# Performance work log

Hardware: AMD Instinct MI355X
Metric: run time of the kernel (lower is better)

Reference implementation:

```python
import jax, jax.numpy as jnp
import numpy as np

NEG_SLOPE_ATT = 0.2   # DenseGATConv default negative_slope
NEG_SLOPE_OUT = 0.01  # F.leaky_relu default


def dense_gat_layer(x, adj, w, att_src, att_dst, bias, heads, concat):
    # x: [B, N, F_in], adj: [B, N, N] (0/1 float), w: [F_in, H*C]
    B, N, _ = x.shape
    h = (x @ w).reshape(B, N, heads, -1)                 # [B, N, H, C]
    a_src = jnp.einsum('bnhc,hc->bnh', h, att_src)       # [B, N, H]
    a_dst = jnp.einsum('bnhc,hc->bnh', h, att_dst)       # [B, N, H]
    # alpha[b,i,j,h] = a_src[b,j,h] + a_dst[b,i,h]
    alpha = a_src[:, None, :, :] + a_dst[:, :, None, :]  # [B, N, N, H]
    alpha = jax.nn.leaky_relu(alpha, NEG_SLOPE_ATT)
    alpha = jnp.where(adj[..., None] == 0, -jnp.inf, alpha)
    alpha = jax.nn.softmax(alpha, axis=2)                # over neighbors j
    out = jnp.einsum('bijh,bjhc->bihc', alpha, h)        # [B, N, H, C]
    if concat:
        out = out.reshape(B, N, -1)                      # [B, N, H*C]
    else:
        out = out.mean(axis=2)                           # [B, N, C]
    return out + bias


def setup_inputs() -> dict:
    key = jax.random.key(0)
    ks = jax.random.split(key, 9)
    B, N, F_IN, HID, H1, OUT = 1, 4096, 256, 64, 8, 128
    x = jax.random.normal(ks[0], (B, N, F_IN), dtype=jnp.float32)
    u = jax.random.uniform(ks[1], (B, N, N), dtype=jnp.float32)
    adj = (u < 0.05).astype(jnp.float32)
    eye = jnp.eye(N, dtype=jnp.float32)[None]
    adj = jnp.maximum(adj, eye)  # ensure self-loop so softmax rows are valid
    s1 = 1.0 / np.sqrt(F_IN)
    s2 = 1.0 / np.sqrt(HID * H1)
    return {
        'x': x,
        'adj': adj,
        'w1': jax.random.normal(ks[2], (F_IN, H1 * HID), dtype=jnp.float32) * s1,
        'att_src1': jax.random.normal(ks[3], (H1, HID), dtype=jnp.float32) * s2,
        'att_dst1': jax.random.normal(ks[4], (H1, HID), dtype=jnp.float32) * s2,
        'b1': jnp.zeros((H1 * HID,), dtype=jnp.float32),
        'w2': jax.random.normal(ks[5], (H1 * HID, OUT), dtype=jnp.float32) * s2,
        'att_src2': jax.random.normal(ks[6], (1, OUT), dtype=jnp.float32) * 0.1,
        'att_dst2': jax.random.normal(ks[7], (1, OUT), dtype=jnp.float32) * 0.1,
        'b2': jnp.zeros((OUT,), dtype=jnp.float32),
    }


def reference(x, adj, w1, att_src1, att_dst1, b1, w2, att_src2, att_dst2, b2):
    h = dense_gat_layer(x, adj, w1, att_src1, att_dst1, b1, heads=8, concat=True)
    h = jax.nn.leaky_relu(h, NEG_SLOPE_OUT)
    h = dense_gat_layer(h, adj, w2, att_src2, att_dst2, b2, heads=1, concat=False)
    return jax.nn.leaky_relu(h, NEG_SLOPE_OUT)
```

## Files before the change

kernel.cpp:

```cpp
#include <hip/hip_runtime.h>
#include <hip/hip_bf16.h>
#include <cstdint>

#define N_NODES 4096
#define STRIDE  384
#define NPAIRS_MAX 192
#define WP1     196
#define QMAX    128

typedef _Float16 half2v __attribute__((ext_vector_type(2)));

__device__ __forceinline__ unsigned pkrtz(float a, float b) {
    return __builtin_bit_cast(unsigned, __builtin_amdgcn_cvt_pkrtz(a, b));
}
__device__ __forceinline__ float f16lo(unsigned u) {
    half2v h = __builtin_bit_cast(half2v, u); return (float)h.x;
}
__device__ __forceinline__ float f16hi(unsigned u) {
    half2v h = __builtin_bit_cast(half2v, u); return (float)h.y;
}
__device__ __forceinline__ unsigned pk_lo(unsigned a, unsigned b) {
    return __builtin_amdgcn_perm(b, a, 0x05040100u);
}
__device__ __forceinline__ unsigned pk_hi(unsigned a, unsigned b) {
    return __builtin_amdgcn_perm(b, a, 0x07060302u);
}
__device__ __forceinline__ float fdot2f(unsigned v, unsigned w, float acc) {
    return __builtin_amdgcn_fdot2(__builtin_bit_cast(half2v, v),
                                  __builtin_bit_cast(half2v, w), acc, false);
}
__device__ __forceinline__ float lrelu02(float s) { return (s > 0.f) ? s : 0.2f * s; }
__device__ __forceinline__ float lrelu01(float s) { return (s > 0.f) ? s : 0.01f * s; }

__global__ __launch_bounds__(256) void build_nbr_kernel(
    const float* __restrict__ adj, unsigned short* __restrict__ nbr,
    int* __restrict__ cnt, float* __restrict__ as1, float* __restrict__ ad1,
    float* __restrict__ as2, float* __restrict__ ad2) {
    const int i    = blockIdx.x;
    const int tid  = threadIdx.x;
    const int wv   = tid >> 6;
    const int lane = tid & 63;
    if (tid < 8)  { as1[i * 8 + tid] = 0.f; ad1[i * 8 + tid] = 0.f; }
    if (tid == 8) { as2[i] = 0.f; }
    if (tid == 9) { ad2[i] = 0.f; }
    __shared__ unsigned short s_buf[4][QMAX];
    __shared__ int s_cnt[4];
    const float4* row = (const float4*)(adj + (size_t)i * N_NODES);
    int base = 0;
#pragma unroll
    for (int it = 0; it < 4; it++) {
        float4 v = row[wv * 256 + it * 64 + lane];
        float e4[4] = {v.x, v.y, v.z, v.w};
        unsigned long long m4[4];
#pragma unroll
        for (int e = 0; e < 4; e++) m4[e] = __ballot(e4[e] != 0.0f);
#pragma unroll
        for (int e = 0; e < 4; e++) {
            int prefix = __popcll(m4[e] & ((1ull << lane) - 1ull));
            int pos = base + prefix;
            if (e4[e] != 0.0f && pos < QMAX)
                s_buf[wv][pos] = (unsigned short)(wv * 1024 + (it * 64 + lane) * 4 + e);
            base += __popcll(m4[e]);
        }
    }
    if (lane == 0) s_cnt[wv] = (base < QMAX) ? base : QMAX;
    __syncthreads();
    const int c0 = s_cnt[0], c1 = s_cnt[1], c2 = s_cnt[2], c3 = s_cnt[3];
    const int o1 = c0, o2 = c0 + c1, o3 = o2 + c2;
    int total = o3 + c3;
    if (total > STRIDE) total = STRIDE;
    for (int k = tid; k < total; k += 256) {
        int w, loc;
        if      (k < o1) { w = 0; loc = k; }
        else if (k < o2) { w = 1; loc = k - o1; }
        else if (k < o3) { w = 2; loc = k - o2; }
        else             { w = 3; loc = k - o3; }
        nbr[(size_t)i * STRIDE + k] = s_buf[w][loc];
    }
    if (tid == 0) cnt[i] = total;
}

template<int BM, int BN, int BK, int TM, int TN, int H>
__global__ __launch_bounds__(256) void sgemm_att_kernel(
    const float* __restrict__ A, const float* __restrict__ B,
    unsigned short* __restrict__ C16,
    const float* __restrict__ att_s, const float* __restrict__ att_d,
    float* __restrict__ as_, float* __restrict__ ad_,
    int M, int N, int K) {
    static_assert((BM / TM) * (BN / TN) == 256, "256 threads");
    static_assert(TN == 4, "epilogue assumes TN=4");
    __shared__ float As[BK][BM + 4];
    __shared__ float Bs[BK][BN + 4];
    const int tid  = threadIdx.x;
    const int tx   = tid % (BN / TN);
    const int ty   = tid / (BN / TN);
    const int row0 = blockIdx.y * BM;
    const int col0 = blockIdx.x * BN;
    float acc[TM][TN] = {};
    for (int k0 = 0; k0 < K; k0 += BK) {
        for (int i = tid; i < BM * BK / 4; i += 256) {
            int r  = i / (BK / 4);
            int kq = i % (BK / 4);
            float4 v = *(const float4*)(A + (size_t)(row0 + r) * K + k0 + kq * 4);
            As[kq * 4 + 0][r] = v.x;
            As[kq * 4 + 1][r] = v.y;
            As[kq * 4 + 2][r] = v.z;
            As[kq * 4 + 3][r] = v.w;
        }
        for (int i = tid; i < BK * BN / 4; i += 256) {
            int r  = i / (BN / 4);
            int cq = i % (BN / 4);
            *(float4*)&Bs[r][cq * 4] =
                *(const float4*)(B + (size_t)(k0 + r) * N + col0 + cq * 4);
        }
        __syncthreads();
#pragma unroll
        for (int kk = 0; kk < BK; kk++) {
            float a[TM], b[TN];
#pragma unroll
            for (int t = 0; t < TM; t++) a[t] = As[kk][ty * TM + t];
#pragma unroll
            for (int u = 0; u < TN; u++) b[u] = Bs[kk][tx * TN + u];
#pragma unroll
            for (int t = 0; t < TM; t++)
#pragma unroll
                for (int u = 0; u < TN; u++) acc[t][u] += a[t] * b[u];
        }
        __syncthreads();
    }
    float asv[TN], adv[TN];
#pragma unroll
    for (int u = 0; u < TN; u++) {
        asv[u] = att_s[col0 + tx * TN + u];
        adv[u] = att_d[col0 + tx * TN + u];
    }
    const int head = (H > 1) ? (col0 >> 6) : 0;
#pragma unroll
    for (int t = 0; t < TM; t++) {
        const int row = row0 + ty * TM + t;
        uint2 pk;
        pk.x = pkrtz(acc[t][0], acc[t][1]);
        pk.y = pkrtz(acc[t][2], acc[t][3]);
        *(uint2*)(C16 + (size_t)row * N + col0 + tx * TN) = pk;
        float ps = 0.f, pd = 0.f;
#pragma unroll
        for (int u = 0; u < TN; u++) { ps += acc[t][u] * asv[u]; pd += acc[t][u] * adv[u]; }
#pragma unroll
        for (int off = 8; off; off >>= 1) {
            ps += __shfl_xor(ps, off);
            pd += __shfl_xor(pd, off);
        }
        if (tx == 0) {
            atomicAdd(&as_[row * H + head], ps);
            atomicAdd(&ad_[row * H + head], pd);
        }
    }
}

__global__ __launch_bounds__(128) void attn1_kernel(
    const unsigned short* __restrict__ h1g, const float* __restrict__ asrc,
    const float* __restrict__ adst, const unsigned short* __restrict__ nbr,
    const int* __restrict__ cnt, const float* __restrict__ b1,
    float* __restrict__ out1) {
    const int wv   = threadIdx.x >> 6;
    const int i    = blockIdx.x * 2 + wv;
    const int lane = threadIdx.x & 63;
    __shared__ __align__(16) unsigned s_wp[2][8][WP1];
    __shared__ __align__(16) unsigned s_nb[2][NPAIRS_MAX];
    __shared__ float s_inv[2][8];

    const int n      = cnt[i];
    const int npairs = (n + 1) >> 1;
    const int nq     = (npairs + 3) >> 2;
    const int npadp  = nq * 4;
    const int npadE  = npadp * 2;

    const unsigned* nbr32 = (const unsigned*)(nbr + (size_t)i * STRIDE);
    for (int k = lane; k < npadp; k += 64) {
        unsigned v = 0u;
        if (2 * k + 1 < n)      v = nbr32[k];
        else if (2 * k < n)     v = nbr32[k] & 0xffffu;
        s_nb[wv][k] = v;
    }

    float ad8[8];
    {
        const float4 a0 = *(const float4*)(adst + i * 8);
        const float4 a1 = *(const float4*)(adst + i * 8 + 4);
        ad8[0]=a0.x; ad8[1]=a0.y; ad8[2]=a0.z; ad8[3]=a0.w;
        ad8[4]=a1.x; ad8[5]=a1.y; ad8[6]=a1.z; ad8[7]=a1.w;
    }
    float m8[8];
#pragma unroll
    for (int k = 0; k < 8; k++) m8[k] = -1e30f;
    for (int e = lane; e < n; e += 64) {
        const int id = (s_nb[wv][e >> 1] >> ((e & 1) * 16)) & 0xffff;
        const float4 q0 = *(const float4*)(asrc + id * 8);
        const float4 q1 = *(const float4*)(asrc + id * 8 + 4);
        const float sv[8] = {q0.x, q0.y, q0.z, q0.w, q1.x, q1.y, q1.z, q1.w};
#pragma unroll
        for (int k = 0; k < 8; k++) m8[k] = fmaxf(m8[k], lrelu02(sv[k] + ad8[k]));
    }
#pragma unroll
    for (int k = 0; k < 8; k++)
#pragma unroll
        for (int off = 32; off; off >>= 1) m8[k] = fmaxf(m8[k], __shfl_xor(m8[k], off));

    float l8[8];
#pragma unroll
    for (int k = 0; k < 8; k++) l8[k] = 0.f;
    unsigned short* wrow = (unsigned short*)&s_wp[wv][0][0];
    for (int e = lane; e < npadE; e += 64) {
        if (e < n) {
            const int id = (s_nb[wv][e >> 1] >> ((e & 1) * 16)) & 0xffff;
            const float4 q0 = *(const float4*)(asrc + id * 8);
            const float4 q1 = *(const float4*)(asrc + id * 8 + 4);
            const float sv[8] = {q0.x, q0.y, q0.z, q0.w, q1.x, q1.y, q1.z, q1.w};
#pragma unroll
            for (int k = 0; k < 8; k++) {
                float ev = __expf(lrelu02(sv[k] + ad8[k]) - m8[k]);
                unsigned h16 = pkrtz(ev, 0.f) & 0xffffu;
                l8[k] += f16lo(h16);
                wrow[k * (WP1 * 2) + e] = (unsigned short)h16;
            }
        } else {
#pragma unroll
            for (int k = 0; k < 8; k++) wrow[k * (WP1 * 2) + e] = 0;
        }
    }
#pragma unroll
    for (int k = 0; k < 8; k++) {
#pragma unroll
        for (int off = 32; off; off >>= 1) l8[k] += __shfl_xor(l8[k], off);
        if (lane == 0) s_inv[wv][k] = 1.0f / l8[k];
    }

    const int hd = lane >> 3;
    const char* hb = (const char*)h1g + lane * 16;
    float ac[8] = {};
    for (int q = 0; q < nq; q++) {
        const uint4 idq = *(const uint4*)&s_nb[wv][q * 4];
        const uint4 wq  = *(const uint4*)&s_wp[wv][hd][q * 4];
        const unsigned idv[4] = {idq.x, idq.y, idq.z, idq.w};
        const unsigned wv4[4] = {wq.x, wq.y, wq.z, wq.w};
#pragma unroll
        for (int p = 0; p < 4; p++) {
            const int iA = idv[p] & 0xffff, iB = idv[p] >> 16;
            const uint4 vA = *(const uint4*)(hb + (size_t)iA * 1024);
            const uint4 vB = *(const uint4*)(hb + (size_t)iB * 1024);
            const unsigned w = wv4[p];
            ac[0] = fdot2f(pk_lo(vA.x, vB.x), w, ac[0]);
            ac[1] = fdot2f(pk_hi(vA.x, vB.x), w, ac[1]);
            ac[2] = fdot2f(pk_lo(vA.y, vB.y), w, ac[2]);
            ac[3] = fdot2f(pk_hi(vA.y, vB.y), w, ac[3]);
            ac[4] = fdot2f(pk_lo(vA.z, vB.z), w, ac[4]);
            ac[5] = fdot2f(pk_hi(vA.z, vB.z), w, ac[5]);
            ac[6] = fdot2f(pk_lo(vA.w, vB.w), w, ac[6]);
            ac[7] = fdot2f(pk_hi(vA.w, vB.w), w, ac[7]);
        }
    }
    const float inv = s_inv[wv][hd];
    const float4 bb0 = *(const float4*)(b1 + lane * 8);
    const float4 bb1 = *(const float4*)(b1 + lane * 8 + 4);
    float4 o0, o1;
    o0.x = lrelu01(ac[0] * inv + bb0.x);
    o0.y = lrelu01(ac[1] * inv + bb0.y);
    o0.z = lrelu01(ac[2] * inv + bb0.z);
    o0.w = lrelu01(ac[3] * inv + bb0.w);
    o1.x = lrelu01(ac[4] * inv + bb1.x);
    o1.y = lrelu01(ac[5] * inv + bb1.y);
    o1.z = lrelu01(ac[6] * inv + bb1.z);
    o1.w = lrelu01(ac[7] * inv + bb1.w);
    *(float4*)(out1 + (size_t)i * 512 + lane * 8)     = o0;
    *(float4*)(out1 + (size_t)i * 512 + lane * 8 + 4) = o1;
}

__global__ __launch_bounds__(128) void attn2_kernel(
    const unsigned short* __restrict__ h2g, const float* __restrict__ asrc,
    const float* __restrict__ adst, const unsigned short* __restrict__ nbr,
    const int* __restrict__ cnt, const float* __restrict__ b2,
    float* __restrict__ out) {
    const int wv   = threadIdx.x >> 6;
    const int i    = blockIdx.x * 2 + wv;
    const int lane = threadIdx.x & 63;
    __shared__ __align__(16) unsigned s_wp[2][WP1];
    __shared__ __align__(16) unsigned s_nb[2][NPAIRS_MAX];

    const int n      = cnt[i];
    const int npairs = (n + 1) >> 1;
    const int nq     = (npairs + 3) >> 2;
    const int npadp  = nq * 4;
    const int npadE  = npadp * 2;

    const unsigned* nbr32 = (const unsigned*)(nbr + (size_t)i * STRIDE);
    for (int k = lane; k < npadp; k += 64) {
        unsigned v = 0u;
        if (2 * k + 1 < n)      v = nbr32[k];
        else if (2 * k < n)     v = nbr32[k] & 0xffffu;
        s_nb[wv][k] = v;
    }

    const float ad = adst[i];
    float sreg[6];
    float m = -1e30f;
    const int niter = (npadE + 63) >> 6;
#pragma unroll 6
    for (int it = 0; it < niter; it++) {
        const int e = it * 64 + lane;
        float s = -1e30f;
        if (e < n) {
            const int id = (s_nb[wv][e >> 1] >> ((e & 1) * 16)) & 0xffff;
            s = lrelu02(asrc[id] + ad);
        }
        sreg[it] = s;
        m = fmaxf(m, s);
    }
#pragma unroll
    for (int off = 32; off; off >>= 1) m = fmaxf(m, __shfl_xor(m, off));
    float l = 0.f;
    unsigned short* wrow = (unsigned short*)&s_wp[wv][0];
#pragma unroll 6
    for (int it = 0; it < niter; it++) {
        const int e = it * 64 + lane;
        if (e < npadE) {
            unsigned h16 = 0u;
            if (e < n) {
                float ev = __expf(sreg[it] - m);
                h16 = pkrtz(ev, 0.f) & 0xffffu;
                l += f16lo(h16);
            }
            wrow[e] = (unsigned short)h16;
        }
    }
#pragma unroll
    for (int off = 32; off; off >>= 1) l += __shfl_xor(l, off);
    const float inv = 1.0f / l;

    const bool hiE = lane >= 32;
    const char* hb = (const char*)h2g + (lane & 31) * 8;
    float a0 = 0.f, a1 = 0.f, a2 = 0.f, a3 = 0.f;
    for (int q = 0; q < nq; q++) {
        const uint4 idq = *(const uint4*)&s_nb[wv][q * 4];
        const uint4 wq  = *(const uint4*)&s_wp[wv][q * 4];
        const unsigned idv[4] = {idq.x, idq.y, idq.z, idq.w};
        const unsigned wv4[4] = {wq.x, wq.y, wq.z, wq.w};
#pragma unroll
        for (int p = 0; p < 4; p++) {
            const unsigned id = hiE ? (idv[p] >> 16) : (idv[p] & 0xffffu);
            const float w = hiE ? f16hi(wv4[p]) : f16lo(wv4[p]);
            const uint2 v = *(const uint2*)(hb + (size_t)id * 256);
            a0 += w * f16lo(v.x);
            a1 += w * f16hi(v.x);
            a2 += w * f16lo(v.y);
            a3 += w * f16hi(v.y);
        }
    }
    a0 += __shfl_xor(a0, 32);
    a1 += __shfl_xor(a1, 32);
    a2 += __shfl_xor(a2, 32);
    a3 += __shfl_xor(a3, 32);
    if (lane < 32) {
        const float4 bb = *(const float4*)(b2 + lane * 4);
        float4 o;
        o.x = lrelu01(a0 * inv + bb.x);
        o.y = lrelu01(a1 * inv + bb.y);
        o.z = lrelu01(a2 * inv + bb.z);
        o.w = lrelu01(a3 * inv + bb.w);
        *(float4*)(out + (size_t)i * 128 + lane * 4) = o;
    }
}

extern "C" void kernel_launch(void* const* d_in, const int* in_sizes, int n_in,
                              void* d_out, int out_size, void* d_ws, size_t ws_size,
                              hipStream_t stream) {
    const float* x        = (const float*)d_in[0];
    const float* adj      = (const float*)d_in[1];
    const float* w1       = (const float*)d_in[2];
    const float* att_src1 = (const float*)d_in[3];
    const float* att_dst1 = (const float*)d_in[4];
    const float* b1       = (const float*)d_in[5];
    const float* w2       = (const float*)d_in[6];
    const float* att_src2 = (const float*)d_in[7];
    const float* att_dst2 = (const float*)d_in[8];
    const float* b2       = (const float*)d_in[9];
    float* out = (float*)d_out;

    float* ws   = (float*)d_ws;
    float* out1 = ws;
    float* as1  = out1 + 4096 * 512;
    float* ad1  = as1 + 4096 * 8;
    float* as2  = ad1 + 4096 * 8;
    float* ad2  = as2 + 4096;
    int*   cnt  = (int*)(ad2 + 4096);
    unsigned short* nbr = (unsigned short*)(cnt + 4096);
    unsigned short* h1g = nbr + (size_t)4096 * STRIDE;
    unsigned short* h2g = h1g + (size_t)4096 * 512;

    build_nbr_kernel<<<N_NODES, 256, 0, stream>>>(adj, nbr, cnt, as1, ad1, as2, ad2);

    sgemm_att_kernel<64, 64, 32, 4, 4, 8>
        <<<dim3(512 / 64, 4096 / 64), 256, 0, stream>>>(
        x, w1, h1g, att_src1, att_dst1, as1, ad1, 4096, 512, 256);
    attn1_kernel<<<N_NODES / 2, 128, 0, stream>>>(h1g, as1, ad1, nbr, cnt, b1, out1);

    sgemm_att_kernel<32, 64, 32, 2, 4, 1>
        <<<dim3(128 / 64, 4096 / 32), 256, 0, stream>>>(
        out1, w2, h2g, att_src2, att_dst2, as2, ad2, 4096, 128, 512);
    attn2_kernel<<<N_NODES / 2, 128, 0, stream>>>(h2g, as2, ad2, nbr, cnt, b2, out);
}
```

Measured before the change: 226.4 us.

## Replace fp32 SGEMMs with fp16 MFMA GEMMs and restructure attention kernels

Adds a prep kernel that converts x to fp16 and writes transposed fp16 copies of the weights, then replaces the LDS-tiled fp32 SGEMMs with per-wave MFMA 16x16x32 f16 GEMMs. Each wave computes full head rows, so the attention-score dot products are stored directly and the atomics and zero-init are gone. Layer-1 output is now stored as fp16, which halves the second GEMM's input traffic but adds precision loss. attn1 splits each node's neighbour loop across two waves combined through LDS, and attn2 gathers 16-byte rows with four edge groups per wave. The extra prep pass and the fp16 rounding are the cost.

```diff
diff --git a/kernel.cpp b/kernel.cpp
--- a/kernel.cpp
+++ b/kernel.cpp
@@ -5,14 +5,14 @@
 #define N_NODES 4096
 #define STRIDE  384
 #define NPAIRS_MAX 192
-#define WP1     196
 #define QMAX    128
+#define WROW    400
 
 typedef _Float16 half2v __attribute__((ext_vector_type(2)));
-
-__device__ __forceinline__ unsigned pkrtz(float a, float b) {
-    return __builtin_bit_cast(unsigned, __builtin_amdgcn_cvt_pkrtz(a, b));
-}
+typedef _Float16 v4h __attribute__((ext_vector_type(4)));
+typedef _Float16 v8h __attribute__((ext_vector_type(8)));
+typedef float    v4f __attribute__((ext_vector_type(4)));
+
 __device__ __forceinline__ float f16lo(unsigned u) {
     half2v h = __builtin_bit_cast(half2v, u); return (float)h.x;
 }
@@ -34,15 +34,11 @@
 
 __global__ __launch_bounds__(256) void build_nbr_kernel(
     const float* __restrict__ adj, unsigned short* __restrict__ nbr,
-    int* __restrict__ cnt, float* __restrict__ as1, float* __restrict__ ad1,
-    float* __restrict__ as2, float* __restrict__ ad2) {
+    int* __restrict__ cnt) {
     const int i    = blockIdx.x;
     const int tid  = threadIdx.x;
     const int wv   = tid >> 6;
     const int lane = tid & 63;
-    if (tid < 8)  { as1[i * 8 + tid] = 0.f; ad1[i * 8 + tid] = 0.f; }
-    if (tid == 8) { as2[i] = 0.f; }
-    if (tid == 9) { ad2[i] = 0.f; }
     __shared__ unsigned short s_buf[4][QMAX];
     __shared__ int s_cnt[4];
     const float4* row = (const float4*)(adj + (size_t)i * N_NODES);
@@ -80,94 +76,94 @@
     if (tid == 0) cnt[i] = total;
 }
 
-template<int BM, int BN, int BK, int TM, int TN, int H>
-__global__ __launch_bounds__(256) void sgemm_att_kernel(
-    const float* __restrict__ A, const float* __restrict__ B,
-    unsigned short* __restrict__ C16,
+__global__ __launch_bounds__(256) void prep_kernel(
+    const float* __restrict__ x, const float* __restrict__ w1,
+    const float* __restrict__ w2, _Float16* __restrict__ x16,
+    _Float16* __restrict__ w1T, _Float16* __restrict__ w2T) {
+    const int b = blockIdx.x, t = threadIdx.x;
+    if (b < 1024) {
+        const int idx = b * 1024 + t * 4;
+        float4 v = *(const float4*)(x + idx);
+        v4h h = { (_Float16)v.x, (_Float16)v.y, (_Float16)v.z, (_Float16)v.w };
+        *(v4h*)(x16 + idx) = h;
+    } else if (b < 1536) {
+        const int idx = (b - 1024) * 256 + t;
+        const int n = idx >> 8, k = idx & 255;
+        w1T[idx] = (_Float16)w1[k * 512 + n];
+    } else {
+        const int idx = (b - 1536) * 256 + t;
+        const int n = idx >> 9, k = idx & 511;
+        w2T[idx] = (_Float16)w2[k * 128 + n];
+    }
+}
+
+template<int KCH, int NSUB, int H>
+__global__ __launch_bounds__(256) void gemm_mfma_kernel(
+    const _Float16* __restrict__ A16, const _Float16* __restrict__ BT16,
+    _Float16* __restrict__ C16,
     const float* __restrict__ att_s, const float* __restrict__ att_d,
-    float* __restrict__ as_, float* __restrict__ ad_,
-    int M, int N, int K) {
-    static_assert((BM / TM) * (BN / TN) == 256, "256 threads");
-    static_assert(TN == 4, "epilogue assumes TN=4");
-    __shared__ float As[BK][BM + 4];
-    __shared__ float Bs[BK][BN + 4];
-    const int tid  = threadIdx.x;
-    const int tx   = tid % (BN / TN);
-    const int ty   = tid / (BN / TN);
-    const int row0 = blockIdx.y * BM;
-    const int col0 = blockIdx.x * BN;
-    float acc[TM][TN] = {};
-    for (int k0 = 0; k0 < K; k0 += BK) {
-        for (int i = tid; i < BM * BK / 4; i += 256) {
-            int r  = i / (BK / 4);
-            int kq = i % (BK / 4);
-            float4 v = *(const float4*)(A + (size_t)(row0 + r) * K + k0 + kq * 4);
-            As[kq * 4 + 0][r] = v.x;
-            As[kq * 4 + 1][r] = v.y;
-            As[kq * 4 + 2][r] = v.z;
-            As[kq * 4 + 3][r] = v.w;
-        }
-        for (int i = tid; i < BK * BN / 4; i += 256) {
-            int r  = i / (BN / 4);
-            int cq = i % (BN / 4);
-            *(float4*)&Bs[r][cq * 4] =
-                *(const float4*)(B + (size_t)(k0 + r) * N + col0 + cq * 4);
-        }
-        __syncthreads();
-#pragma unroll
-        for (int kk = 0; kk < BK; kk++) {
-            float a[TM], b[TN];
-#pragma unroll
-            for (int t = 0; t < TM; t++) a[t] = As[kk][ty * TM + t];
-#pragma unroll
-            for (int u = 0; u < TN; u++) b[u] = Bs[kk][tx * TN + u];
-#pragma unroll
-            for (int t = 0; t < TM; t++)
-#pragma unroll
-                for (int u = 0; u < TN; u++) acc[t][u] += a[t] * b[u];
-        }
-        __syncthreads();
-    }
-    float asv[TN], adv[TN];
-#pragma unroll
-    for (int u = 0; u < TN; u++) {
-        asv[u] = att_s[col0 + tx * TN + u];
-        adv[u] = att_d[col0 + tx * TN + u];
-    }
-    const int head = (H > 1) ? (col0 >> 6) : 0;
-#pragma unroll
-    for (int t = 0; t < TM; t++) {
-        const int row = row0 + ty * TM + t;
-        uint2 pk;
-        pk.x = pkrtz(acc[t][0], acc[t][1]);
-        pk.y = pkrtz(acc[t][2], acc[t][3]);
-        *(uint2*)(C16 + (size_t)row * N + col0 + tx * TN) = pk;
-        float ps = 0.f, pd = 0.f;
-#pragma unroll
-        for (int u = 0; u < TN; u++) { ps += acc[t][u] * asv[u]; pd += acc[t][u] * adv[u]; }
-#pragma unroll
-        for (int off = 8; off; off >>= 1) {
-            ps += __shfl_xor(ps, off);
-            pd += __shfl_xor(pd, off);
-        }
-        if (tx == 0) {
-            atomicAdd(&as_[row * H + head], ps);
-            atomicAdd(&ad_[row * H + head], pd);
+    float* __restrict__ as_, float* __restrict__ ad_, int N) {
+    const int K    = KCH * 32;
+    const int wid  = blockIdx.x * 4 + (threadIdx.x >> 6);
+    const int lane = threadIdx.x & 63;
+    const int quad = lane >> 4, l16 = lane & 15;
+    const int ntiles = N / (16 * NSUB);
+    const int m0 = (wid / ntiles) * 16;
+    const int n0 = (wid % ntiles) * (16 * NSUB);
+
+    v8h a[KCH];
+    const v8h* arow = (const v8h*)(A16 + (size_t)(m0 + l16) * K + quad * 8);
+#pragma unroll
+    for (int c = 0; c < KCH; c++) a[c] = arow[c * 4];
+
+    float ps[4] = {}, pd[4] = {};
+#pragma unroll
+    for (int s = 0; s < NSUB; s++) {
+        const int n = n0 + s * 16 + l16;
+        const v8h* brow = (const v8h*)(BT16 + (size_t)n * K + quad * 8);
+        v4f acc = {0.f, 0.f, 0.f, 0.f};
+#pragma unroll
+        for (int c = 0; c < KCH; c++)
+            acc = __builtin_amdgcn_mfma_f32_16x16x32_f16(a[c], brow[c * 4], acc, 0, 0, 0);
+        const float sa = att_s[n], sd = att_d[n];
+#pragma unroll
+        for (int r = 0; r < 4; r++) {
+            C16[(size_t)(m0 + quad * 4 + r) * N + n] = (_Float16)acc[r];
+            ps[r] += acc[r] * sa;
+            pd[r] += acc[r] * sd;
+        }
+    }
+#pragma unroll
+    for (int r = 0; r < 4; r++) {
+#pragma unroll
+        for (int off = 1; off < 16; off <<= 1) {
+            ps[r] += __shfl_xor(ps[r], off);
+            pd[r] += __shfl_xor(pd[r], off);
+        }
+    }
+    if (l16 == 0) {
+        const int head = (H > 1) ? (n0 >> 6) : 0;
+#pragma unroll
+        for (int r = 0; r < 4; r++) {
+            const int row = m0 + quad * 4 + r;
+            as_[row * H + head] = ps[r];
+            ad_[row * H + head] = pd[r];
         }
     }
 }
 
 __global__ __launch_bounds__(128) void attn1_kernel(
-    const unsigned short* __restrict__ h1g, const float* __restrict__ asrc,
+    const _Float16* __restrict__ h1g, const float* __restrict__ asrc,
     const float* __restrict__ adst, const unsigned short* __restrict__ nbr,
     const int* __restrict__ cnt, const float* __restrict__ b1,
-    float* __restrict__ out1) {
+    _Float16* __restrict__ out1f16) {
+    const int i    = blockIdx.x;
     const int wv   = threadIdx.x >> 6;
-    const int i    = blockIdx.x * 2 + wv;
     const int lane = threadIdx.x & 63;
-    __shared__ __align__(16) unsigned s_wp[2][8][WP1];
-    __shared__ __align__(16) unsigned s_nb[2][NPAIRS_MAX];
-    __shared__ float s_inv[2][8];
+    const int hd   = lane >> 3;
+    __shared__ __align__(16) unsigned s_nb[NPAIRS_MAX];
+    __shared__ __align__(16) unsigned short s_w16[8][WROW];
+    __shared__ __align__(16) float s_comb[512];
 
     const int n      = cnt[i];
     const int npairs = (n + 1) >> 1;
@@ -178,9 +174,9 @@
     const unsigned* nbr32 = (const unsigned*)(nbr + (size_t)i * STRIDE);
     for (int k = lane; k < npadp; k += 64) {
         unsigned v = 0u;
-        if (2 * k + 1 < n)      v = nbr32[k];
-        else if (2 * k < n)     v = nbr32[k] & 0xffffu;
-        s_nb[wv][k] = v;
+        if (2 * k + 1 < n)  v = nbr32[k];
+        else if (2 * k < n) v = nbr32[k] & 0xffffu;
+        s_nb[k] = v;
     }
 
     float ad8[8];
@@ -194,7 +190,7 @@
 #pragma unroll
     for (int k = 0; k < 8; k++) m8[k] = -1e30f;
     for (int e = lane; e < n; e += 64) {
-        const int id = (s_nb[wv][e >> 1] >> ((e & 1) * 16)) & 0xffff;
+        const int id = (s_nb[e >> 1] >> ((e & 1) * 16)) & 0xffff;
         const float4 q0 = *(const float4*)(asrc + id * 8);
         const float4 q1 = *(const float4*)(asrc + id * 8 + 4);
         const float sv[8] = {q0.x, q0.y, q0.z, q0.w, q1.x, q1.y, q1.z, q1.w};
@@ -209,38 +205,34 @@
     float l8[8];
 #pragma unroll
     for (int k = 0; k < 8; k++) l8[k] = 0.f;
-    unsigned short* wrow = (unsigned short*)&s_wp[wv][0][0];
     for (int e = lane; e < npadE; e += 64) {
         if (e < n) {
-            const int id = (s_nb[wv][e >> 1] >> ((e & 1) * 16)) & 0xffff;
+            const int id = (s_nb[e >> 1] >> ((e & 1) * 16)) & 0xffff;
             const float4 q0 = *(const float4*)(asrc + id * 8);
             const float4 q1 = *(const float4*)(asrc + id * 8 + 4);
             const float sv[8] = {q0.x, q0.y, q0.z, q0.w, q1.x, q1.y, q1.z, q1.w};
 #pragma unroll
             for (int k = 0; k < 8; k++) {
                 float ev = __expf(lrelu02(sv[k] + ad8[k]) - m8[k]);
-                unsigned h16 = pkrtz(ev, 0.f) & 0xffffu;
-                l8[k] += f16lo(h16);
-                wrow[k * (WP1 * 2) + e] = (unsigned short)h16;
+                _Float16 h = (_Float16)ev;
+                l8[k] += (float)h;
+                s_w16[k][e] = __builtin_bit_cast(unsigned short, h);
             }
         } else {
 #pragma unroll
-            for (int k = 0; k < 8; k++) wrow[k * (WP1 * 2) + e] = 0;
-        }
-    }
-#pragma unroll
-    for (int k = 0; k < 8; k++) {
+            for (int k = 0; k < 8; k++) s_w16[k][e] = 0;
+        }
+    }
+#pragma unroll
+    for (int k = 0; k < 8; k++)
 #pragma unroll
         for (int off = 32; off; off >>= 1) l8[k] += __shfl_xor(l8[k], off);
-        if (lane == 0) s_inv[wv][k] = 1.0f / l8[k];
-    }
-
-    const int hd = lane >> 3;
+
     const char* hb = (const char*)h1g + lane * 16;
     float ac[8] = {};
-    for (int q = 0; q < nq; q++) {
-        const uint4 idq = *(const uint4*)&s_nb[wv][q * 4];
-        const uint4 wq  = *(const uint4*)&s_wp[wv][hd][q * 4];
+    for (int q = wv; q < nq; q += 2) {
+        const uint4 idq = *(const uint4*)&s_nb[q * 4];
+        const uint4 wq  = *(const uint4*)((const unsigned*)&s_w16[hd][0] + q * 4);
         const unsigned idv[4] = {idq.x, idq.y, idq.z, idq.w};
         const unsigned wv4[4] = {wq.x, wq.y, wq.z, wq.w};
 #pragma unroll
@@ -259,53 +251,61 @@
             ac[7] = fdot2f(pk_hi(vA.w, vB.w), w, ac[7]);
         }
     }
-    const float inv = s_inv[wv][hd];
-    const float4 bb0 = *(const float4*)(b1 + lane * 8);
-    const float4 bb1 = *(const float4*)(b1 + lane * 8 + 4);
-    float4 o0, o1;
-    o0.x = lrelu01(ac[0] * inv + bb0.x);
-    o0.y = lrelu01(ac[1] * inv + bb0.y);
-    o0.z = lrelu01(ac[2] * inv + bb0.z);
-    o0.w = lrelu01(ac[3] * inv + bb0.w);
-    o1.x = lrelu01(ac[4] * inv + bb1.x);
-    o1.y = lrelu01(ac[5] * inv + bb1.y);
-    o1.z = lrelu01(ac[6] * inv + bb1.z);
-    o1.w = lrelu01(ac[7] * inv + bb1.w);
-    *(float4*)(out1 + (size_t)i * 512 + lane * 8)     = o0;
-    *(float4*)(out1 + (size_t)i * 512 + lane * 8 + 4) = o1;
+    if (wv == 0) {
+        *(float4*)&s_comb[lane * 8]     = make_float4(ac[0], ac[1], ac[2], ac[3]);
+        *(float4*)&s_comb[lane * 8 + 4] = make_float4(ac[4], ac[5], ac[6], ac[7]);
+    }
+    __syncthreads();
+    if (wv == 1) {
+        const float4 c0 = *(const float4*)&s_comb[lane * 8];
+        const float4 c1 = *(const float4*)&s_comb[lane * 8 + 4];
+        ac[0] += c0.x; ac[1] += c0.y; ac[2] += c0.z; ac[3] += c0.w;
+        ac[4] += c1.x; ac[5] += c1.y; ac[6] += c1.z; ac[7] += c1.w;
+        float lv = (hd < 4)
+            ? ((hd < 2) ? (hd == 0 ? l8[0] : l8[1]) : (hd == 2 ? l8[2] : l8[3]))
+            : ((hd < 6) ? (hd == 4 ? l8[4] : l8[5]) : (hd == 6 ? l8[6] : l8[7]));
+        const float inv = 1.0f / lv;
+        const float4 bb0 = *(const float4*)(b1 + lane * 8);
+        const float4 bb1 = *(const float4*)(b1 + lane * 8 + 4);
+        const float bbv[8] = {bb0.x, bb0.y, bb0.z, bb0.w, bb1.x, bb1.y, bb1.z, bb1.w};
+        v8h ov;
+#pragma unroll
+        for (int c = 0; c < 8; c++)
+            ov[c] = (_Float16)lrelu01(ac[c] * inv + bbv[c]);
+        *(v8h*)(out1f16 + (size_t)i * 512 + lane * 8) = ov;
+    }
 }
 
 __global__ __launch_bounds__(128) void attn2_kernel(
-    const unsigned short* __restrict__ h2g, const float* __restrict__ asrc,
+    const _Float16* __restrict__ h2g, const float* __restrict__ asrc,
     const float* __restrict__ adst, const unsigned short* __restrict__ nbr,
     const int* __restrict__ cnt, const float* __restrict__ b2,
     float* __restrict__ out) {
     const int wv   = threadIdx.x >> 6;
     const int i    = blockIdx.x * 2 + wv;
     const int lane = threadIdx.x & 63;
-    __shared__ __align__(16) unsigned s_wp[2][WP1];
+    const int grp  = lane >> 4, l16 = lane & 15;
     __shared__ __align__(16) unsigned s_nb[2][NPAIRS_MAX];
-
-    const int n      = cnt[i];
-    const int npairs = (n + 1) >> 1;
-    const int nq     = (npairs + 3) >> 2;
-    const int npadp  = nq * 4;
-    const int npadE  = npadp * 2;
+    __shared__ __align__(16) unsigned short s_w16[2][STRIDE + 16];
+
+    const int n     = cnt[i];
+    const int nq4   = (n + 3) >> 2;
+    const int npad4 = nq4 * 4;
+    const int npadp = (npad4 + 1) >> 1;
 
     const unsigned* nbr32 = (const unsigned*)(nbr + (size_t)i * STRIDE);
     for (int k = lane; k < npadp; k += 64) {
         unsigned v = 0u;
-        if (2 * k + 1 < n)      v = nbr32[k];
-        else if (2 * k < n)     v = nbr32[k] & 0xffffu;
+        if (2 * k + 1 < n)  v = nbr32[k];
+        else if (2 * k < n) v = nbr32[k] & 0xffffu;
         s_nb[wv][k] = v;
     }
 
     const float ad = adst[i];
     float sreg[6];
     float m = -1e30f;
-    const int niter = (npadE + 63) >> 6;
-#pragma unroll 6
-    for (int it = 0; it < niter; it++) {
+#pragma unroll
+    for (int it = 0; it < 6; it++) {
         const int e = it * 64 + lane;
         float s = -1e30f;
         if (e < n) {
@@ -318,55 +318,53 @@
 #pragma unroll
     for (int off = 32; off; off >>= 1) m = fmaxf(m, __shfl_xor(m, off));
     float l = 0.f;
-    unsigned short* wrow = (unsigned short*)&s_wp[wv][0];
-#pragma unroll 6
-    for (int it = 0; it < niter; it++) {
+#pragma unroll
+    for (int it = 0; it < 6; it++) {
         const int e = it * 64 + lane;
-        if (e < npadE) {
-            unsigned h16 = 0u;
-            if (e < n) {
-                float ev = __expf(sreg[it] - m);
-                h16 = pkrtz(ev, 0.f) & 0xffffu;
-                l += f16lo(h16);
-            }
-            wrow[e] = (unsigned short)h16;
-        }
-    }
+        if (e < n) {
+            float ev = __expf(sreg[it] - m);
+            _Float16 h = (_Float16)ev;
+            l += (float)h;
+            s_w16[wv][e] = __builtin_bit_cast(unsigned short, h);
+        }
+    }
+    if (lane < npad4 - n) s_w16[wv][n + lane] = 0;
 #pragma unroll
     for (int off = 32; off; off >>= 1) l += __shfl_xor(l, off);
     const float inv = 1.0f / l;
 
-    const bool hiE = lane >= 32;
-    const char* hb = (const char*)h2g + (lane & 31) * 8;
-    float a0 = 0.f, a1 = 0.f, a2 = 0.f, a3 = 0.f;
-    for (int q = 0; q < nq; q++) {
-        const uint4 idq = *(const uint4*)&s_nb[wv][q * 4];
-        const uint4 wq  = *(const uint4*)&s_wp[wv][q * 4];
-        const unsigned idv[4] = {idq.x, idq.y, idq.z, idq.w};
-        const unsigned wv4[4] = {wq.x, wq.y, wq.z, wq.w};
-#pragma unroll
-        for (int p = 0; p < 4; p++) {
-            const unsigned id = hiE ? (idv[p] >> 16) : (idv[p] & 0xffffu);
-            const float w = hiE ? f16hi(wv4[p]) : f16lo(wv4[p]);
-            const uint2 v = *(const uint2*)(hb + (size_t)id * 256);
-            a0 += w * f16lo(v.x);
-            a1 += w * f16hi(v.x);
-            a2 += w * f16lo(v.y);
-            a3 += w * f16hi(v.y);
-        }
-    }
-    a0 += __shfl_xor(a0, 32);
-    a1 += __shfl_xor(a1, 32);
-    a2 += __shfl_xor(a2, 32);
-    a3 += __shfl_xor(a3, 32);
-    if (lane < 32) {
-        const float4 bb = *(const float4*)(b2 + lane * 4);
-        float4 o;
-        o.x = lrelu01(a0 * inv + bb.x);
-        o.y = lrelu01(a1 * inv + bb.y);
-        o.z = lrelu01(a2 * inv + bb.z);
-        o.w = lrelu01(a3 * inv + bb.w);
-        *(float4*)(out + (size_t)i * 128 + lane * 4) = o;
+    const char* hb = (const char*)h2g + l16 * 16;
+    float ac[8] = {};
+    for (int it = 0; it < nq4; it++) {
+        const int e = it * 4 + grp;
+        const unsigned pr = s_nb[wv][e >> 1];
+        const int id = (e & 1) ? (int)(pr >> 16) : (int)(pr & 0xffffu);
+        const float w = (float)((const _Float16*)&s_w16[wv][0])[e];
+        const uint4 v = *(const uint4*)(hb + (size_t)id * 256);
+        ac[0] += w * f16lo(v.x); ac[1] += w * f16hi(v.x);
+        ac[2] += w * f16lo(v.y); ac[3] += w * f16hi(v.y);
+        ac[4] += w * f16lo(v.z); ac[5] += w * f16hi(v.z);
+        ac[6] += w * f16lo(v.w); ac[7] += w * f16hi(v.w);
+    }
+#pragma unroll
+    for (int c = 0; c < 8; c++) {
+        ac[c] += __shfl_xor(ac[c], 16);
+        ac[c] += __shfl_xor(ac[c], 32);
+    }
+    if (lane < 16) {
+        const float4 bb0 = *(const float4*)(b2 + lane * 8);
+        const float4 bb1 = *(const float4*)(b2 + lane * 8 + 4);
+        float4 o0, o1;
+        o0.x = lrelu01(ac[0] * inv + bb0.x);
+        o0.y = lrelu01(ac[1] * inv + bb0.y);
+        o0.z = lrelu01(ac[2] * inv + bb0.z);
+        o0.w = lrelu01(ac[3] * inv + bb0.w);
+        o1.x = lrelu01(ac[4] * inv + bb1.x);
+        o1.y = lrelu01(ac[5] * inv + bb1.y);
+        o1.z = lrelu01(ac[6] * inv + bb1.z);
+        o1.w = lrelu01(ac[7] * inv + bb1.w);
+        *(float4*)(out + (size_t)i * 128 + lane * 8)     = o0;
+        *(float4*)(out + (size_t)i * 128 + lane * 8 + 4) = o1;
     }
 }
 
@@ -386,25 +384,27 @@
     float* out = (float*)d_out;
 
     float* ws   = (float*)d_ws;
-    float* out1 = ws;
-    float* as1  = out1 + 4096 * 512;
+    float* as1  = ws;
     float* ad1  = as1 + 4096 * 8;
     float* as2  = ad1 + 4096 * 8;
     float* ad2  = as2 + 4096;
     int*   cnt  = (int*)(ad2 + 4096);
-    unsigned short* nbr = (unsigned short*)(cnt + 4096);
-    unsigned short* h1g = nbr + (size_t)4096 * STRIDE;
-    unsigned short* h2g = h1g + (size_t)4096 * 512;
-
-    build_nbr_kernel<<<N_NODES, 256, 0, stream>>>(adj, nbr, cnt, as1, ad1, as2, ad2);
-
-    sgemm_att_kernel<64, 64, 32, 4, 4, 8>
-        <<<dim3(512 / 64, 4096 / 64), 256, 0, stream>>>(
-        x, w1, h1g, att_src1, att_dst1, as1, ad1, 4096, 512, 256);
-    attn1_kernel<<<N_NODES / 2, 128, 0, stream>>>(h1g, as1, ad1, nbr, cnt, b1, out1);
-
-    sgemm_att_kernel<32, 64, 32, 2, 4, 1>
-        <<<dim3(128 / 64, 4096 / 32), 256, 0, stream>>>(
-        out1, w2, h2g, att_src2, att_dst2, as2, ad2, 4096, 128, 512);
+    _Float16* x16   = (_Float16*)(cnt + 4096);
+    _Float16* w1T   = x16 + (size_t)4096 * 256;
+    _Float16* w2T   = w1T + 512 * 256;
+    _Float16* h1g   = w2T + 128 * 512;
+    _Float16* out1h = h1g + (size_t)4096 * 512;
+    _Float16* h2g   = out1h + (size_t)4096 * 512;
+    unsigned short* nbr = (unsigned short*)(h2g + (size_t)4096 * 128);
+
+    build_nbr_kernel<<<N_NODES, 256, 0, stream>>>(adj, nbr, cnt);
+    prep_kernel<<<1792, 256, 0, stream>>>(x, w1, w2, x16, w1T, w2T);
+
+    gemm_mfma_kernel<8, 4, 8><<<512, 256, 0, stream>>>(
+        x16, w1T, h1g, att_src1, att_dst1, as1, ad1, 512);
+    attn1_kernel<<<N_NODES, 128, 0, stream>>>(h1g, as1, ad1, nbr, cnt, b1, out1h);
+
+    gemm_mfma_kernel<16, 8, 1><<<64, 256, 0, stream>>>(
+        out1h, w2T, h2g, att_src2, att_dst2, as2, ad2, 128);
     attn2_kernel<<<N_NODES / 2, 128, 0, stream>>>(h2g, as2, ad2, nbr, cnt, b2, out);
 }
```

After: 217.0 us. 4.1% less time.
